# Optimization experiments

Hardware: AMD Instinct MI355X
Metric: run time of the kernel (lower is better)

Reference implementation:

```python
import jax, jax.numpy as jnp
import numpy as np

CONF_THRES = 0.25
IOU_THRES = 0.45
MAX_ANCHORS = 50
PRE_NMS_TOPK = 2048   # candidate cap, standard fused-NMS trick to bound the IoU matrix
NEG = -1.0e9
NUM_CLASSES = 80
IMG = 640.0


def setup_inputs() -> dict:
    key = jax.random.key(0)
    k1, k2, k3, k4 = jax.random.split(key, 4)
    B, N = 16, 25200
    # realistic xyxy boxes inside a 640x640 image
    cxcy = jax.random.uniform(k1, (B, N, 2), minval=0.0, maxval=IMG)
    wh = jax.random.uniform(k2, (B, N, 2), minval=4.0, maxval=64.0)
    x1y1 = jnp.clip(cxcy - 0.5 * wh, 0.0, IMG)
    x2y2 = jnp.clip(cxcy + 0.5 * wh, 0.0, IMG)
    conf = jax.random.uniform(k3, (B, N, 1))
    cls = jax.random.randint(k4, (B, N, 1), 0, NUM_CLASSES).astype(jnp.float32)
    x = jnp.concatenate([x1y1, x2y2, conf, cls], axis=-1)  # [B, N, 6]
    return {"x": x}


def _box_iou_matrix(boxes):
    # boxes: [K, 4] xyxy -> [K, K] pairwise IoU
    x1, y1, x2, y2 = boxes[:, 0], boxes[:, 1], boxes[:, 2], boxes[:, 3]
    area = jnp.maximum(x2 - x1, 0.0) * jnp.maximum(y2 - y1, 0.0)  # [K]
    iw = jnp.maximum(jnp.minimum(x2[:, None], x2[None, :]) - jnp.maximum(x1[:, None], x1[None, :]), 0.0)
    ih = jnp.maximum(jnp.minimum(y2[:, None], y2[None, :]) - jnp.maximum(y1[:, None], y1[None, :]), 0.0)
    inter = iw * ih
    union = area[:, None] + area[None, :] - inter
    return inter / jnp.maximum(union, 1e-9)


def _nms_single(bx):
    # bx: [N, 6] -> [MAX_ANCHORS, 6], rows padded with -1 (keep_shape semantics)
    scores = bx[:, 4]
    s = jnp.where(scores > CONF_THRES, scores, NEG)  # confidence filter
    top_s, top_i = jax.lax.top_k(s, PRE_NMS_TOPK)     # sort descending by score
    cand = jnp.take(bx, top_i, axis=0)                # [K, 6]
    cvalid = top_s > 0.5 * NEG                        # passed conf filter

    iou = _box_iou_matrix(cand[:, :4])                # [K, K]
    idxs = jnp.arange(PRE_NMS_TOPK)
    # box i may only suppress lower-scored boxes j > i
    suppr_rows = (iou >= IOU_THRES) & (idxs[None, :] > idxs[:, None])

    def step(suppressed, i):
        keep_i = cvalid[i] & jnp.logical_not(suppressed[i])
        suppressed = suppressed | (keep_i & suppr_rows[i])
        return suppressed, keep_i

    _, keep = jax.lax.scan(step, jnp.zeros(PRE_NMS_TOPK, dtype=bool), idxs)

    final_s = jnp.where(keep, cand[:, 4], NEG)
    sel_s, sel_i = jax.lax.top_k(final_s, MAX_ANCHORS)  # top-50 kept boxes by conf
    rows = jnp.take(cand, sel_i, axis=0)                # [50, 6]
    return jnp.where((sel_s > 0.5 * NEG)[:, None], rows, -1.0)


def reference(x):
    # x: [B, N, 6] -> [B, MAX_ANCHORS, 6]
    return jax.vmap(_nms_single)(x)
```

## Files before the change

kernel.cpp:

```cpp
#include <hip/hip_runtime.h>

#define BATCH   16
#define NANCH   25200
#define TPB     1024
#define MAXK    50
#define PRETOPK 2048
#define CONF_T  0.25f
#define IOU_T   0.45f
#define NEGV    -1000000000.0f
#define NBINS   4096
#define CHUNK   256

__device__ __forceinline__ int bin_of(float s) {
    int b = (int)((s - CONF_T) * ((float)NBINS / 0.75f));
    return b > (NBINS - 1) ? (NBINS - 1) : b;
}

__global__ __launch_bounds__(TPB, 1) void nms_kernel(const float* __restrict__ x,
                                                     float* __restrict__ out) {
    __shared__ float s_scores[NANCH];
    __shared__ unsigned int s_hist[NBINS];
    __shared__ unsigned long long s_keys[CHUNK];
    __shared__ float s_srows[CHUNK][8];
    __shared__ int s_hi, s_c, s_cnt, s_nk, s_P;

    const int b    = blockIdx.x;
    const int tid  = threadIdx.x;
    const int lane = tid & 63;
    const int wave = tid >> 6;

    const float* __restrict__ xb = x + (size_t)b * NANCH * 6;
    float* __restrict__ ob       = out + (size_t)b * MAXK * 6;

    for (int i = tid; i < NBINS; i += TPB) s_hist[i] = 0u;
    if (tid == 0) { s_hi = NBINS; s_nk = 0; s_P = 0; }
    __syncthreads();

    for (int i = tid; i < NANCH; i += TPB) {
        float s = xb[(size_t)i * 6 + 4];
        bool valid = s > CONF_T;
        s_scores[i] = valid ? s : NEGV;
        if (valid) atomicAdd(&s_hist[bin_of(s)], 1u);
    }
    __syncthreads();

    float kx1 = 0.f, ky1 = 0.f, kx2 = 0.f, ky2 = 0.f, ka = 0.f;
    int nk = 0;

    while (s_nk < MAXK && s_P < PRETOPK && s_hi > 0) {
        if (wave == 0) {
            int c = s_hi;
            int room = CHUNK;
            while (c > 0) {
                int nb = c < 64 ? c : 64;
                unsigned cnt = (lane < nb) ? s_hist[c - 1 - lane] : 0u;
                unsigned pre = cnt;
                #pragma unroll
                for (int o = 1; o < 64; o <<= 1) {
                    unsigned t = __shfl_up(pre, o);
                    if (lane >= o) pre += t;
                }
                unsigned total = __shfl(pre, 63);
                if (total <= (unsigned)room) { room -= (int)total; c -= nb; continue; }
                unsigned long long m = __ballot((lane < nb) && (pre <= (unsigned)room));
                int n = __popcll(m);
                if (n == 0 && room == CHUNK) n = 1;
                c -= n;
                break;
            }
            if (lane == 0) s_c = c;
        } else {
            int z = tid - 64;
            if (z < CHUNK) s_keys[z] = 0ULL;
            if (z == CHUNK) s_cnt = 0;
        }
        __syncthreads();

        const int c = s_c, hi = s_hi;

        for (int i = tid; i < NANCH; i += TPB) {
            float s = s_scores[i];
            if (s > CONF_T) {
                int bn = bin_of(s);
                if (bn >= c && bn < hi) {
                    int slot = atomicAdd(&s_cnt, 1);
                    if (slot < CHUNK) {
                        s_keys[slot] =
                            ((unsigned long long)__float_as_uint(s) << 32) |
                            ((unsigned long long)(65535 - i) << 16) |
                            (unsigned long long)slot;
                    }
                }
            }
        }
        __syncthreads();

        const int K = (s_cnt < CHUNK) ? s_cnt : CHUNK;

        if (tid < CHUNK) {
            const unsigned long long mykey = s_keys[tid];
            float2 r0, r1, r2;
            int myi = 0;
            const bool real = tid < K;
            if (real) {
                myi = 65535 - (int)((mykey >> 16) & 0xFFFFULL);
                const float2* rp = (const float2*)(xb + (size_t)myi * 6);
                r0 = rp[0]; r1 = rp[1]; r2 = rp[2];
            }
            int r = 0;
            #pragma unroll 4
            for (int j = 0; j < CHUNK; ++j) r += (s_keys[j] > mykey) ? 1 : 0;
            if (real) {
                s_srows[r][0] = r0.x; s_srows[r][1] = r0.y;
                s_srows[r][2] = r1.x; s_srows[r][3] = r1.y;
                s_srows[r][4] = r2.x; s_srows[r][5] = r2.y;
            }
        }
        __syncthreads();

        if (wave == 0) {
            const int rem   = PRETOPK - s_P;
            const int Kproc = K < rem ? K : rem;
            float4 nb0 = {0, 0, 0, 0}; float2 nb1 = {0, 0};
            if (Kproc > 0) {
                nb0 = *(const float4*)&s_srows[0][0];
                nb1 = *(const float2*)&s_srows[0][4];
            }
            for (int ii = 0; ii < Kproc && nk < MAXK; ++ii) {
                const float4 cb0 = nb0; const float2 cb1 = nb1;
                if (ii + 1 < Kproc) {
                    nb0 = *(const float4*)&s_srows[ii + 1][0];
                    nb1 = *(const float2*)&s_srows[ii + 1][4];
                }
                const float ba = fmaxf(cb0.z - cb0.x, 0.0f) * fmaxf(cb0.w - cb0.y, 0.0f);
                bool sup = false;
                if (lane < nk) {
                    float iw = fmaxf(fminf(cb0.z, kx2) - fmaxf(cb0.x, kx1), 0.0f);
                    float ih = fmaxf(fminf(cb0.w, ky2) - fmaxf(cb0.y, ky1), 0.0f);
                    float inter = iw * ih;
                    float uni   = ba + ka - inter;
                    sup = (inter / fmaxf(uni, 1e-9f)) >= IOU_T;
                }
                if (__ballot(sup) == 0ULL) {
                    if (lane == nk) {
                        kx1 = cb0.x; ky1 = cb0.y; kx2 = cb0.z; ky2 = cb0.w; ka = ba;
                        ob[nk * 6 + 0] = cb0.x;
                        ob[nk * 6 + 1] = cb0.y;
                        ob[nk * 6 + 2] = cb0.z;
                        ob[nk * 6 + 3] = cb0.w;
                        ob[nk * 6 + 4] = cb1.x;
                        ob[nk * 6 + 5] = cb1.y;
                    }
                    ++nk;
                }
            }
            if (lane == 0) { s_nk = nk; s_P = s_P + Kproc; s_hi = s_c; }
        }
        __syncthreads();
    }

    const int nkf = s_nk;
    for (int i = tid; i < (MAXK - nkf) * 6; i += TPB) {
        ob[nkf * 6 + i] = -1.0f;
    }
}

extern "C" void kernel_launch(void* const* d_in, const int* in_sizes, int n_in,
                              void* d_out, int out_size, void* d_ws, size_t ws_size,
                              hipStream_t stream) {
    const float* x = (const float*)d_in[0];
    float* out     = (float*)d_out;
    nms_kernel<<<BATCH, TPB, 0, stream>>>(x, out);
}
```

Baseline: 31.39 us.

## Process NMS candidates in 64-wide tiles with bitmask intra-tile suppression

Replaces the one-candidate-per-iteration greedy NMS loop, where each step needs a wave ballot, with a tiled scheme. Each lane takes one candidate from a 64-candidate tile and tests it against all kept boxes, which are now stored in shared memory. It then builds an intra-tile overlap bitmask, and a short ballot loop resolves greedy order within the tile. This cuts the serial dependency chain per candidate, at the cost of computing IoU against all 64 tile members even when few survive.

```diff
diff --git a/kernel.cpp b/kernel.cpp
--- a/kernel.cpp
+++ b/kernel.cpp
@@ -22,6 +22,7 @@
     __shared__ unsigned int s_hist[NBINS];
     __shared__ unsigned long long s_keys[CHUNK];
     __shared__ float s_srows[CHUNK][8];
+    __shared__ float s_kx1[MAXK], s_ky1[MAXK], s_kx2[MAXK], s_ky2[MAXK], s_ka[MAXK];
     __shared__ int s_hi, s_c, s_cnt, s_nk, s_P;
 
     const int b    = blockIdx.x;
@@ -43,9 +44,6 @@
         if (valid) atomicAdd(&s_hist[bin_of(s)], 1u);
     }
     __syncthreads();
-
-    float kx1 = 0.f, ky1 = 0.f, kx2 = 0.f, ky2 = 0.f, ka = 0.f;
-    int nk = 0;
 
     while (s_nk < MAXK && s_P < PRETOPK && s_hi > 0) {
         if (wave == 0) {
@@ -100,10 +98,9 @@
         if (tid < CHUNK) {
             const unsigned long long mykey = s_keys[tid];
             float2 r0, r1, r2;
-            int myi = 0;
             const bool real = tid < K;
             if (real) {
-                myi = 65535 - (int)((mykey >> 16) & 0xFFFFULL);
+                int myi = 65535 - (int)((mykey >> 16) & 0xFFFFULL);
                 const float2* rp = (const float2*)(xb + (size_t)myi * 6);
                 r0 = rp[0]; r1 = rp[1]; r2 = rp[2];
             }
@@ -121,37 +118,61 @@
         if (wave == 0) {
             const int rem   = PRETOPK - s_P;
             const int Kproc = K < rem ? K : rem;
-            float4 nb0 = {0, 0, 0, 0}; float2 nb1 = {0, 0};
-            if (Kproc > 0) {
-                nb0 = *(const float4*)&s_srows[0][0];
-                nb1 = *(const float2*)&s_srows[0][4];
-            }
-            for (int ii = 0; ii < Kproc && nk < MAXK; ++ii) {
-                const float4 cb0 = nb0; const float2 cb1 = nb1;
-                if (ii + 1 < Kproc) {
-                    nb0 = *(const float4*)&s_srows[ii + 1][0];
-                    nb1 = *(const float2*)&s_srows[ii + 1][4];
+            int nk = s_nk;
+
+            for (int tb = 0; tb < Kproc && nk < MAXK; tb += 64) {
+                const int lim = (Kproc - tb) < 64 ? (Kproc - tb) : 64;
+                float4 bx = {0.f, 0.f, 0.f, 0.f};
+                float2 be = {0.f, 0.f};
+                bool sup = lane >= lim;
+                if (!sup) {
+                    bx = *(const float4*)&s_srows[tb + lane][0];
+                    be = *(const float2*)&s_srows[tb + lane][4];
                 }
-                const float ba = fmaxf(cb0.z - cb0.x, 0.0f) * fmaxf(cb0.w - cb0.y, 0.0f);
-                bool sup = false;
-                if (lane < nk) {
-                    float iw = fmaxf(fminf(cb0.z, kx2) - fmaxf(cb0.x, kx1), 0.0f);
-                    float ih = fmaxf(fminf(cb0.w, ky2) - fmaxf(cb0.y, ky1), 0.0f);
+                const float ba = fmaxf(bx.z - bx.x, 0.f) * fmaxf(bx.w - bx.y, 0.f);
+
+                for (int j = 0; j < nk; ++j) {
+                    float iw = fmaxf(fminf(bx.z, s_kx2[j]) - fmaxf(bx.x, s_kx1[j]), 0.f);
+                    float ih = fmaxf(fminf(bx.w, s_ky2[j]) - fmaxf(bx.y, s_ky1[j]), 0.f);
                     float inter = iw * ih;
-                    float uni   = ba + ka - inter;
-                    sup = (inter / fmaxf(uni, 1e-9f)) >= IOU_T;
+                    sup = sup || (inter / fmaxf(ba + s_ka[j] - inter, 1e-9f)) >= IOU_T;
                 }
-                if (__ballot(sup) == 0ULL) {
-                    if (lane == nk) {
-                        kx1 = cb0.x; ky1 = cb0.y; kx2 = cb0.z; ky2 = cb0.w; ka = ba;
-                        ob[nk * 6 + 0] = cb0.x;
-                        ob[nk * 6 + 1] = cb0.y;
-                        ob[nk * 6 + 2] = cb0.z;
-                        ob[nk * 6 + 3] = cb0.w;
-                        ob[nk * 6 + 4] = cb1.x;
-                        ob[nk * 6 + 5] = cb1.y;
-                    }
+
+                unsigned long long m = 0ULL;
+                #pragma unroll 8
+                for (int j = 0; j < 64; ++j) {
+                    if (j >= lim) break;
+                    const float4 oj = *(const float4*)&s_srows[tb + j][0];
+                    const float oa = fmaxf(oj.z - oj.x, 0.f) * fmaxf(oj.w - oj.y, 0.f);
+                    float iw = fmaxf(fminf(bx.z, oj.z) - fmaxf(bx.x, oj.x), 0.f);
+                    float ih = fmaxf(fminf(bx.w, oj.w) - fmaxf(bx.y, oj.y), 0.f);
+                    float inter = iw * ih;
+                    bool ov = (inter / fmaxf(ba + oa - inter, 1e-9f)) >= IOU_T;
+                    m |= ov ? (1ULL << j) : 0ULL;
+                }
+                m &= ~(1ULL << lane);
+
+                unsigned long long alive = __ballot(!sup);
+                unsigned long long keepmask = 0ULL;
+                while (alive != 0ULL && nk < MAXK) {
+                    const int j = __builtin_ctzll(alive);
+                    keepmask |= 1ULL << j;
                     ++nk;
+                    const unsigned long long kill = __ballot((m >> j) & 1ULL);
+                    alive &= ~(kill | (1ULL << j));
+                }
+
+                if ((keepmask >> lane) & 1ULL) {
+                    const int nk0 = nk - __popcll(keepmask);
+                    const int pos = nk0 + __popcll(keepmask & ((1ULL << lane) - 1ULL));
+                    s_kx1[pos] = bx.x; s_ky1[pos] = bx.y;
+                    s_kx2[pos] = bx.z; s_ky2[pos] = bx.w; s_ka[pos] = ba;
+                    ob[pos * 6 + 0] = bx.x;
+                    ob[pos * 6 + 1] = bx.y;
+                    ob[pos * 6 + 2] = bx.z;
+                    ob[pos * 6 + 3] = bx.w;
+                    ob[pos * 6 + 4] = be.x;
+                    ob[pos * 6 + 5] = be.y;
                 }
             }
             if (lane == 0) { s_nk = nk; s_P = s_P + Kproc; s_hi = s_c; }
```

New measurement: 28.16 us. 10.3% less time.
